# Performance work log

Hardware: AMD Instinct MI355X
Metric: run time of the kernel (lower is better)

## Reference

```python
import jax, jax.numpy as jnp
import numpy as np

MODEL_DIM = 2048
NUM_HEADS = 16
NUM_KV_HEADS = 4
HEAD_DIM = MODEL_DIM // NUM_HEADS  # 128
ROPE_BASE = 10000.0
LOCAL_WINDOW = 1024
EPS = 1.1920929e-07  # torch.finfo(float32).eps, F.rms_norm default
NEG = -1e30


def setup_inputs() -> dict:
    key = jax.random.key(0)
    ks = jax.random.split(key, 5)
    s = 0.02
    return {
        "x": jax.random.normal(ks[0], (1, 4096, MODEL_DIM), jnp.float32),
        "Wq": jax.random.normal(ks[1], (MODEL_DIM, MODEL_DIM), jnp.float32) * s,
        "Wk": jax.random.normal(ks[2], (NUM_KV_HEADS * HEAD_DIM, MODEL_DIM), jnp.float32) * s,
        "Wv": jax.random.normal(ks[3], (NUM_KV_HEADS * HEAD_DIM, MODEL_DIM), jnp.float32) * s,
        "Wo": jax.random.normal(ks[4], (MODEL_DIM, MODEL_DIM), jnp.float32) * s,
    }


def _rms_norm(x):
    return x * jax.lax.rsqrt(jnp.mean(x * x, axis=-1, keepdims=True) + EPS)


def _rope_tables(seqlen, dtype):
    inv_freq = 1.0 / (ROPE_BASE ** (jnp.arange(0, HEAD_DIM, 2, dtype=jnp.float32) / HEAD_DIM))
    freqs = jnp.arange(seqlen, dtype=jnp.float32)[:, None] * inv_freq[None, :]  # [S, hd/2]
    return jnp.cos(freqs).astype(dtype), jnp.sin(freqs).astype(dtype)


def _apply_rope(x, cos, sin):
    # x: [B, H, S, hd]; cos/sin: [S, hd/2]
    half = x.shape[-1] // 2
    x1, x2 = x[..., :half], x[..., half:]
    c = cos[None, None, :, :]
    s = sin[None, None, :, :]
    return jnp.concatenate((x1 * c + x2 * s, x2 * c - x1 * s), axis=-1)


def reference(x, Wq, Wk, Wv, Wo):
    B, S, _ = x.shape
    G = NUM_HEADS // NUM_KV_HEADS
    q = (x @ Wq.T).reshape(B, S, NUM_HEADS, HEAD_DIM).transpose(0, 2, 1, 3)
    k = (x @ Wk.T).reshape(B, S, NUM_KV_HEADS, HEAD_DIM).transpose(0, 2, 1, 3)
    v = (x @ Wv.T).reshape(B, S, NUM_KV_HEADS, HEAD_DIM).transpose(0, 2, 1, 3)
    q = _rms_norm(q)
    k = _rms_norm(k)
    cos, sin = _rope_tables(S, q.dtype)
    q = _apply_rope(q, cos, sin)
    k = _apply_rope(k, cos, sin)
    # GQA: expand kv heads to match query heads
    k = jnp.repeat(k, G, axis=1)  # [B, H, S, hd]
    v = jnp.repeat(v, G, axis=1)
    scale = 1.0 / np.sqrt(HEAD_DIM)
    scores = jnp.einsum("bhqd,bhkd->bhqk", q, k) * scale  # [B, H, S, S]
    idx = jnp.arange(S)
    causal = idx[None, :] <= idx[:, None]
    in_window = idx[None, :] > idx[:, None] - LOCAL_WINDOW
    allowed = causal & in_window  # [S, S]
    scores = jnp.where(allowed[None, None, :, :], scores, NEG)
    probs = jax.nn.softmax(scores, axis=-1)
    y = jnp.einsum("bhqk,bhkd->bhqd", probs, v)  # [B, H, S, hd]
    y = y.transpose(0, 2, 1, 3).reshape(B, S, MODEL_DIM)
    return y @ Wo.T
```

## Files before the change

### kernel.cpp

```cpp
#include <hip/hip_runtime.h>

typedef short bf16x8 __attribute__((ext_vector_type(8)));
typedef float f32x4 __attribute__((ext_vector_type(4)));

__device__ __forceinline__ ushort f2b(float f) {
  union { float f; unsigned u; } v; v.f = f;
  unsigned r = v.u + 0x7FFF + ((v.u >> 16) & 1);
  return (ushort)(r >> 16);
}
__device__ __forceinline__ float b2f(ushort u) {
  union { unsigned u; float f; } v; v.u = ((unsigned)u) << 16;
  return v.f;
}
__device__ __forceinline__ unsigned cvtpk(float lo, float hi) {
  unsigned r;
  asm volatile("v_cvt_pk_bf16_f32 %0, %1, %2" : "=v"(r) : "v"(lo), "v"(hi));
  return r;
}
__device__ __forceinline__ f32x4 mfma16(bf16x8 a, bf16x8 b, f32x4 c) {
  return __builtin_amdgcn_mfma_f32_16x16x32_bf16(a, b, c, 0, 0, 0);
}

#define GLD_LDS16(g, l) \
  __builtin_amdgcn_global_load_lds((const __attribute__((address_space(1))) void*)(g), \
                                   (__attribute__((address_space(3))) void*)(l), 16, 0, 0)

__global__ __launch_bounds__(256) void cast_bf16(const float* __restrict__ in,
                                                 ushort* __restrict__ out, int n4) {
  int i = blockIdx.x * 256 + threadIdx.x;
  if (i >= n4) return;
  float4 f = ((const float4*)in)[i];
  ushort4 u;
  u.x = f2b(f.x); u.y = f2b(f.y); u.z = f2b(f.z); u.w = f2b(f.w);
  ((ushort4*)out)[i] = u;
}

__global__ void rope_tables_k(float* __restrict__ cosT, float* __restrict__ sinT) {
  int s = blockIdx.x, i = threadIdx.x;
  float inv = powf(10000.0f, -(float)i * (1.0f / 64.0f));
  float f = (float)s * inv;
  cosT[s * 64 + i] = cosf(f);
  sinT[s * 64 + i] = sinf(f);
}

template <int BM, int BN, bool BF16OUT>
__global__ __launch_bounds__(512, 2) void gemm8p(const ushort* __restrict__ A,
                                                 const ushort* __restrict__ B,
                                                 void* __restrict__ Cout,
                                                 int M, int N, int K) {
  constexpr int AF = BM / 64;
  constexpr int BF = BN / 64;
  constexpr int MFR = BM / 32;
  constexpr int LA = BM / 128;
  constexpr int LB = BN / 128;
  constexpr int ASZ = BM * 32;
  constexpr int BSZ = BN * 32;
  __shared__ __align__(16) ushort lds[4 * (ASZ + BSZ)];
  const int t = threadIdx.x;
  const int lane = t & 63, w = t >> 6;
  const int wr = w & 1, wc = w >> 1;
  const int l15 = lane & 15, l4 = lane >> 4;
  const int nbn = N / BN;
  const int nwg = (int)gridDim.x;
  int bid = (int)blockIdx.x;
  bid = (bid & 7) * (nwg >> 3) + (bid >> 3);
  const long m0 = (long)(bid / nbn) * BM;
  const long n0 = (long)(bid % nbn) * BN;
  const int nk = K >> 6;
  const int rdl = (l4 * 16 + l15) * 8;

  f32x4 acc[MFR][BF] = {};
  bf16x8 af[AF], bf[BF];

#define STA(tile, ks)                                                          \
  do {                                                                         \
    const int tt_ = (tile) < nk ? (tile) : nk - 1;                             \
    _Pragma("unroll") for (int c = 0; c < LA; ++c) {                           \
      const int us_ = t * 8 + c * 4096;                                        \
      const int row_ = (us_ >> 9) * 16 + ((us_ >> 3) & 15);                    \
      const int col_ = ((us_ >> 7) & 3) * 8;                                   \
      GLD_LDS16(A + (m0 + row_) * K + tt_ * 64 + (ks) * 32 + col_,             \
                &lds[(((tile) & 1) * 2 + (ks)) * ASZ + us_]);                  \
    }                                                                          \
  } while (0)
#define STB(tile, ks)                                                          \
  do {                                                                         \
    const int tt_ = (tile) < nk ? (tile) : nk - 1;                             \
    _Pragma("unroll") for (int c = 0; c < LB; ++c) {                           \
      const int us_ = t * 8 + c * 4096;                                        \
      const int row_ = (us_ >> 9) * 16 + ((us_ >> 3) & 15);                    \
      const int col_ = ((us_ >> 7) & 3) * 8;                                   \
      GLD_LDS16(B + (n0 + row_) * K + tt_ * 64 + (ks) * 32 + col_,             \
                &lds[4 * ASZ + (((tile) & 1) * 2 + (ks)) * BSZ + us_]);        \
    }                                                                          \
  } while (0)
#define LDA8(slot, ks, mq)                                                     \
  _Pragma("unroll") for (int a = 0; a < AF; ++a)                               \
      af[a] = *(const bf16x8*)(&lds[((slot) * 2 + (ks)) * ASZ +                \
                                    (wr * MFR + (mq) * AF + a) * 512 + rdl]);
#define LDB8(slot, ks)                                                         \
  _Pragma("unroll") for (int b = 0; b < BF; ++b)                               \
      bf[b] = *(const bf16x8*)(&lds[4 * ASZ + ((slot) * 2 + (ks)) * BSZ +      \
                                    (wc * BF + b) * 512 + rdl]);
#define VMW()                                                                  \
  do {                                                                         \
    if constexpr (LA + 2 * LB == 6)                                            \
      asm volatile("s_waitcnt vmcnt(6)" ::: "memory");                         \
    else                                                                       \
      asm volatile("s_waitcnt vmcnt(5)" ::: "memory");                         \
  } while (0)
#define BARMM(mq)                                                              \
  do {                                                                         \
    __builtin_amdgcn_s_barrier();                                              \
    asm volatile("s_waitcnt lgkmcnt(0)" ::: "memory");                         \
    __builtin_amdgcn_sched_barrier(0);                                         \
    __builtin_amdgcn_s_setprio(1);                                             \
    _Pragma("unroll") for (int a = 0; a < AF; ++a)                             \
        _Pragma("unroll") for (int b = 0; b < BF; ++b)                         \
            acc[(mq) * AF + a][b] = mfma16(af[a], bf[b], acc[(mq) * AF + a][b]); \
    __builtin_amdgcn_s_setprio(0);                                             \
    __builtin_amdgcn_s_barrier();                                              \
  } while (0)

  STA(0, 0); STB(0, 0); STA(0, 1); STB(0, 1);
  STA(1, 0); STB(1, 0); STB(1, 1);
  VMW();
  __builtin_amdgcn_s_barrier();

  for (int i = 0; i < (nk >> 1); ++i) {
    const int t1 = 2 * i + 1, t2 = 2 * i + 2, t3 = 2 * i + 3;
    LDA8(0, 0, 0); LDB8(0, 0); STA(t1, 1);          BARMM(0);
    LDA8(0, 0, 1);             STB(t2, 0);          BARMM(1);
    LDA8(0, 1, 0); LDB8(0, 1); STA(t2, 0);          BARMM(0);
    LDA8(0, 1, 1);             STB(t2, 1); VMW();   BARMM(1);
    LDA8(1, 0, 0); LDB8(1, 0); STA(t2, 1);          BARMM(0);
    LDA8(1, 0, 1);             STB(t3, 0);          BARMM(1);
    LDA8(1, 1, 0); LDB8(1, 1); STA(t3, 0);          BARMM(0);
    LDA8(1, 1, 1);             STB(t3, 1); VMW();   BARMM(1);
  }
  asm volatile("s_waitcnt vmcnt(0)" ::: "memory");

#pragma unroll
  for (int m = 0; m < MFR; ++m) {
#pragma unroll
    for (int n = 0; n < BF; ++n) {
      long mrow = m0 + wr * (BM / 2) + m * 16 + l4 * 4;
      long ncol = n0 + wc * (BN / 4) + n * 16 + l15;
#pragma unroll
      for (int r = 0; r < 4; ++r) {
        if constexpr (BF16OUT)
          ((ushort*)Cout)[(mrow + r) * N + ncol] = f2b(acc[m][n][r]);
        else
          ((float*)Cout)[(mrow + r) * N + ncol] = acc[m][n][r];
      }
    }
  }
#undef STA
#undef STB
#undef LDA8
#undef LDB8
#undef VMW
#undef BARMM
}

__global__ __launch_bounds__(256) void postproc_k(const ushort* __restrict__ qkvb,
                                                  const float* __restrict__ cosT,
                                                  const float* __restrict__ sinT,
                                                  ushort* __restrict__ qb,
                                                  ushort* __restrict__ kb,
                                                  ushort* __restrict__ vtb) {
  const int lane = threadIdx.x & 63;
  const int s = blockIdx.x * 4 + (threadIdx.x >> 6);
  const int h = blockIdx.y;
  const int colbase = (h < 16) ? h * 128 : (h < 20 ? 2048 + (h - 16) * 128
                                                   : 2560 + (h - 20) * 128);
  const ushort* row = qkvb + (long)s * 3072 + colbase;
  float x1 = b2f(row[lane]), x2 = b2f(row[lane + 64]);
  if (h >= 20) {
    int kvh = h - 20;
    int spos = (s & ~31) | (((s >> 2) & 3) * 8 + ((s >> 4) & 1) * 4 + (s & 3));
    vtb[(long)(kvh * 128 + lane) * 4096 + spos]      = f2b(x1);
    vtb[(long)(kvh * 128 + lane + 64) * 4096 + spos] = f2b(x2);
    return;
  }
  float ss = x1 * x1 + x2 * x2;
#pragma unroll
  for (int m = 1; m < 64; m <<= 1) ss += __shfl_xor(ss, m);
  float rn = rsqrtf(ss * (1.0f / 128.0f) + 1.1920929e-07f);
  float c = cosT[s * 64 + lane], sn = sinT[s * 64 + lane];
  float x1n = x1 * rn, x2n = x2 * rn;
  float o1 = x1n * c + x2n * sn;
  float o2 = x2n * c - x1n * sn;
  if (h < 16) {
    const float scq = 0.08838834764831845f;
    ushort* dst = qb + ((long)h * 4096 + s) * 128;
    dst[lane] = f2b(o1 * scq);
    dst[lane + 64] = f2b(o2 * scq);
  } else {
    ushort* dst = kb + ((long)(h - 16) * 4096 + s) * 128;
    dst[lane] = f2b(o1);
    dst[lane + 64] = f2b(o2);
  }
}

__global__ __launch_bounds__(512) void attn_k(const ushort* __restrict__ qb,
                                              const ushort* __restrict__ kb,
                                              const ushort* __restrict__ vtb,
                                              ushort* __restrict__ yb) {
  __shared__ __align__(16) ushort lds[32768];
  const int t = threadIdx.x;
  const int lane = t & 63, w = t >> 6;
  const int l15 = lane & 15, l4 = lane >> 4;
  const int q0 = ((int)gridDim.x - 1 - (int)blockIdx.x) * 128;
  const int h = blockIdx.y, kvh = h >> 2;
  const int qw = q0 + w * 16;
  const int q = qw + l15;

  const ushort* Qp = qb + ((long)h * 4096 + q) * 128 + l4 * 8;
  bf16x8 qf[4];
#pragma unroll
  for (int c = 0; c < 4; ++c) qf[c] = *(const bf16x8*)(Qp + c * 32);

  const ushort* Kg = kb + (long)kvh * 4096 * 128;
  const ushort* Vg = vtb + (long)kvh * 128 * 4096;

  int kb_lo = q0 - 1023; if (kb_lo < 0) kb_lo = 0; kb_lo &= ~63;
  const int nt = (q0 + 127 - kb_lo) / 64 + 1;

  const int lbuA = w * 512 + lane * 8;
  const int lbuB = lbuA + 4096;
  const int krA = ((lbuA >> 9) >> 2) * 16 + ((lbuA >> 3) & 15);
  const int kcA = ((lbuA >> 9) & 3) * 32 + ((lbuA >> 7) & 3) * 8;
  const int krB = ((lbuB >> 9) >> 2) * 16 + ((lbuB >> 3) & 15);
  const int kcB = ((lbuB >> 9) & 3) * 32 + ((lbuB >> 7) & 3) * 8;
  const int vrA = ((lbuA >> 9) >> 1) * 16 + ((lbuA >> 5) & 15);
  const int vcA = ((lbuA >> 9) & 1) * 32 + ((lbuA >> 3) & 3) * 8;
  const int vrB = ((lbuB >> 9) >> 1) * 16 + ((lbuB >> 5) & 15);
  const int vcB = ((lbuB >> 9) & 1) * 32 + ((lbuB >> 3) & 3) * 8;

#define STAGE(kbs, b)                                                        \
  do {                                                                       \
    ushort* Kl_ = &lds[(b) * 16384];                                         \
    ushort* Vl_ = &lds[(b) * 16384 + 8192];                                  \
    GLD_LDS16(Kg + (long)((kbs) + krA) * 128 + kcA, Kl_ + lbuA);             \
    GLD_LDS16(Kg + (long)((kbs) + krB) * 128 + kcB, Kl_ + lbuB);             \
    GLD_LDS16(Vg + (long)vrA * 4096 + (kbs) + vcA, Vl_ + lbuA);              \
    GLD_LDS16(Vg + (long)vrB * 4096 + (kbs) + vcB, Vl_ + lbuB);              \
  } while (0)

  f32x4 o[8] = {};
  float mrun = -1e30f, lrun = 0.0f;

  STAGE(kb_lo, 0);
  asm volatile("s_waitcnt vmcnt(0)" ::: "memory");
  __syncthreads();

  for (int ti = 0; ti < nt; ++ti) {
    const int kbs = kb_lo + ti * 64;
    const int cur = ti & 1;
    if (ti + 1 < nt) STAGE(kbs + 64, cur ^ 1);

    if (kbs + 63 >= qw - 1023 && kbs <= qw + 15) {
      const ushort* Kl = &lds[cur * 16384];
      const ushort* Vl = &lds[cur * 16384 + 8192];
      const int rdl = (l4 * 16 + l15) * 8;

      f32x4 sc[4];
#pragma unroll
      for (int st = 0; st < 4; ++st) {
        sc[st] = f32x4{0.f, 0.f, 0.f, 0.f};
#pragma unroll
        for (int c = 0; c < 4; ++c)
          sc[st] = mfma16(*(const bf16x8*)(Kl + (st * 4 + c) * 512 + rdl),
                          qf[c], sc[st]);
      }

      const bool full = (kbs + 64 <= qw) && (kbs >= qw - 1008);
      float s[16];
      if (full) {
#pragma unroll
        for (int st = 0; st < 4; ++st)
#pragma unroll
          for (int r = 0; r < 4; ++r) s[st * 4 + r] = sc[st][r];
      } else {
#pragma unroll
        for (int st = 0; st < 4; ++st)
#pragma unroll
          for (int r = 0; r < 4; ++r) {
            const int ki = kbs + st * 16 + l4 * 4 + r;
            s[st * 4 + r] = (ki <= q && ki > q - 1024) ? sc[st][r] : -1e30f;
          }
      }

      float m0a = fmaxf(fmaxf(s[0], s[1]), fmaxf(s[2], s[3]));
      float m1a = fmaxf(fmaxf(s[4], s[5]), fmaxf(s[6], s[7]));
      float m2a = fmaxf(fmaxf(s[8], s[9]), fmaxf(s[10], s[11]));
      float m3a = fmaxf(fmaxf(s[12], s[13]), fmaxf(s[14], s[15]));
      float mx = fmaxf(fmaxf(m0a, m1a), fmaxf(m2a, m3a));
      mx = fmaxf(mx, __shfl_xor(mx, 16));
      mx = fmaxf(mx, __shfl_xor(mx, 32));

      float mn;
      if (__all(mx <= mrun + 8.0f)) {
        mn = mrun;
      } else {
        mn = fmaxf(mrun, mx);
        const float corr = __expf(mrun - mn);
        mrun = mn;
#pragma unroll
        for (int db = 0; db < 8; ++db)
#pragma unroll
          for (int r = 0; r < 4; ++r) o[db][r] *= corr;
        lrun *= corr;
      }

      float p[16];
#pragma unroll
      for (int j = 0; j < 16; ++j) p[j] = __expf(s[j] - mn);
      float ps = ((p[0] + p[1]) + (p[2] + p[3])) + ((p[4] + p[5]) + (p[6] + p[7]));
      ps += ((p[8] + p[9]) + (p[10] + p[11])) + ((p[12] + p[13]) + (p[14] + p[15]));
      ps += __shfl_xor(ps, 16);
      ps += __shfl_xor(ps, 32);
      lrun += ps;

      union { unsigned u[4]; bf16x8 v; } pa, pb;
      pa.u[0] = cvtpk(p[0], p[1]);   pa.u[1] = cvtpk(p[2], p[3]);
      pa.u[2] = cvtpk(p[4], p[5]);   pa.u[3] = cvtpk(p[6], p[7]);
      pb.u[0] = cvtpk(p[8], p[9]);   pb.u[1] = cvtpk(p[10], p[11]);
      pb.u[2] = cvtpk(p[12], p[13]); pb.u[3] = cvtpk(p[14], p[15]);

      const int vbase = l15 * 32 + l4 * 8;
#pragma unroll
      for (int db = 0; db < 8; ++db) {
        const ushort* vrp = Vl + db * 1024 + vbase;
        o[db] = mfma16(*(const bf16x8*)vrp, pa.v, o[db]);
        o[db] = mfma16(*(const bf16x8*)(vrp + 512), pb.v, o[db]);
      }
    }
    __syncthreads();
  }

  const float inv = 1.0f / lrun;
#pragma unroll
  for (int db = 0; db < 8; ++db)
#pragma unroll
    for (int r = 0; r < 4; ++r)
      yb[(long)q * 2048 + h * 128 + db * 16 + l4 * 4 + r] = f2b(o[db][r] * inv);
}

extern "C" void kernel_launch(void* const* d_in, const int* in_sizes, int n_in,
                              void* d_out, int out_size, void* d_ws, size_t ws_size,
                              hipStream_t stream) {
  (void)in_sizes; (void)n_in; (void)out_size; (void)ws_size;
  const float* x  = (const float*)d_in[0];
  const float* Wq = (const float*)d_in[1];
  const float* Wk = (const float*)d_in[2];
  const float* Wv = (const float*)d_in[3];
  const float* Wo = (const float*)d_in[4];
  const long S = 4096;
  ushort* ws   = (ushort*)d_ws;
  ushort* xb   = ws;
  ushort* wqkv = xb + S * 2048;
  ushort* wob  = wqkv + 3072L * 2048;
  ushort* qkvb = wob + 2048L * 2048;
  ushort* qb   = qkvb + S * 3072;
  ushort* kbuf = qb + S * 2048;
  ushort* vtb  = kbuf + 4L * 4096 * 128;
  ushort* yb   = vtb + 4L * 128 * 4096;
  float* cosT  = (float*)(yb + S * 2048);
  float* sinT  = cosT + S * 64;

  cast_bf16<<<dim3(8192), 256, 0, stream>>>(x, xb, (int)(S * 2048 / 4));
  cast_bf16<<<dim3(4096), 256, 0, stream>>>(Wq, wqkv, 2048 * 2048 / 4);
  cast_bf16<<<dim3(1024), 256, 0, stream>>>(Wk, wqkv + 2048L * 2048, 512 * 2048 / 4);
  cast_bf16<<<dim3(1024), 256, 0, stream>>>(Wv, wqkv + 2560L * 2048, 512 * 2048 / 4);
  cast_bf16<<<dim3(4096), 256, 0, stream>>>(Wo, wob, 2048 * 2048 / 4);

  gemm8p<256, 256, true><<<dim3(192), 512, 0, stream>>>(xb, wqkv, qkvb, 4096, 3072, 2048);
  rope_tables_k<<<dim3(4096), 64, 0, stream>>>(cosT, sinT);
  postproc_k<<<dim3(1024, 24), 256, 0, stream>>>(qkvb, cosT, sinT, qb, kbuf, vtb);
  attn_k<<<dim3(32, 16), 512, 0, stream>>>(qb, kbuf, vtb, yb);
  gemm8p<128, 256, false><<<dim3(256), 512, 0, stream>>>(yb, wob, d_out, 4096, 2048, 2048);
}
```

Measured before the change: 225.1 us.

## Fuse casts, simplify GEMM LDS layout, process two query tiles per attention wave

The five fp32-to-bf16 cast launches become one kernel that branches on index range, removing launch overhead. The GEMM global-to-LDS staging switches to a plain row-major 32-column layout with matching fragment read offsets. The attention kernel now runs 4 waves of 256 threads, each handling 32 queries as two 16-row groups. Each K/V fragment read from LDS therefore feeds two MFMAs, and two blocks per CU are requested. This doubles per-wave accumulator registers and may add LDS bank conflicts from the simpler layout.

New measurement: 201.6 us. 10.4% less time.

```diff
diff --git a/kernel.cpp b/kernel.cpp
--- a/kernel.cpp
+++ b/kernel.cpp
@@ -25,14 +25,33 @@
   __builtin_amdgcn_global_load_lds((const __attribute__((address_space(1))) void*)(g), \
                                    (__attribute__((address_space(3))) void*)(l), 16, 0, 0)
 
-__global__ __launch_bounds__(256) void cast_bf16(const float* __restrict__ in,
-                                                 ushort* __restrict__ out, int n4) {
-  int i = blockIdx.x * 256 + threadIdx.x;
-  if (i >= n4) return;
-  float4 f = ((const float4*)in)[i];
+__global__ __launch_bounds__(256) void cast_all(const float* __restrict__ x,
+                                                const float* __restrict__ wq,
+                                                const float* __restrict__ wk,
+                                                const float* __restrict__ wv,
+                                                const float* __restrict__ wo,
+                                                ushort* __restrict__ xb,
+                                                ushort* __restrict__ wqkvb,
+                                                ushort* __restrict__ wob) {
+  const long i = (long)blockIdx.x * 256 + threadIdx.x;
+  const float* src;
+  ushort* dst;
+  long j;
+  if (i < 2097152) {
+    src = x; j = i; dst = xb;
+  } else if (i < 3145728) {
+    src = wq; j = i - 2097152; dst = wqkvb;
+  } else if (i < 3407872) {
+    src = wk; j = i - 3145728; dst = wqkvb + 4194304;
+  } else if (i < 3670016) {
+    src = wv; j = i - 3407872; dst = wqkvb + 5242880;
+  } else {
+    src = wo; j = i - 3670016; dst = wob;
+  }
+  float4 f = ((const float4*)src)[j];
   ushort4 u;
   u.x = f2b(f.x); u.y = f2b(f.y); u.z = f2b(f.z); u.w = f2b(f.w);
-  ((ushort4*)out)[i] = u;
+  ((ushort4*)dst)[j] = u;
 }
 
 __global__ void rope_tables_k(float* __restrict__ cosT, float* __restrict__ sinT) {
@@ -67,7 +86,7 @@
   const long m0 = (long)(bid / nbn) * BM;
   const long n0 = (long)(bid % nbn) * BN;
   const int nk = K >> 6;
-  const int rdl = (l4 * 16 + l15) * 8;
+  const int rdl = l15 * 32 + l4 * 8;
 
   f32x4 acc[MFR][BF] = {};
   bf16x8 af[AF], bf[BF];
@@ -77,9 +96,7 @@
     const int tt_ = (tile) < nk ? (tile) : nk - 1;                             \
     _Pragma("unroll") for (int c = 0; c < LA; ++c) {                           \
       const int us_ = t * 8 + c * 4096;                                        \
-      const int row_ = (us_ >> 9) * 16 + ((us_ >> 3) & 15);                    \
-      const int col_ = ((us_ >> 7) & 3) * 8;                                   \
-      GLD_LDS16(A + (m0 + row_) * K + tt_ * 64 + (ks) * 32 + col_,             \
+      GLD_LDS16(A + (m0 + (us_ >> 5)) * K + tt_ * 64 + (ks) * 32 + (us_ & 31), \
                 &lds[(((tile) & 1) * 2 + (ks)) * ASZ + us_]);                  \
     }                                                                          \
   } while (0)
@@ -88,9 +105,7 @@
     const int tt_ = (tile) < nk ? (tile) : nk - 1;                             \
     _Pragma("unroll") for (int c = 0; c < LB; ++c) {                           \
       const int us_ = t * 8 + c * 4096;                                        \
-      const int row_ = (us_ >> 9) * 16 + ((us_ >> 3) & 15);                    \
-      const int col_ = ((us_ >> 7) & 3) * 8;                                   \
-      GLD_LDS16(B + (n0 + row_) * K + tt_ * 64 + (ks) * 32 + col_,             \
+      GLD_LDS16(B + (n0 + (us_ >> 5)) * K + tt_ * 64 + (ks) * 32 + (us_ & 31), \
                 &lds[4 * ASZ + (((tile) & 1) * 2 + (ks)) * BSZ + us_]);        \
     }                                                                          \
   } while (0)
@@ -203,23 +218,30 @@
   }
 }
 
-__global__ __launch_bounds__(512) void attn_k(const ushort* __restrict__ qb,
-                                              const ushort* __restrict__ kb,
-                                              const ushort* __restrict__ vtb,
-                                              ushort* __restrict__ yb) {
+__global__ __launch_bounds__(256, 2) void attn_k(const ushort* __restrict__ qb,
+                                                 const ushort* __restrict__ kb,
+                                                 const ushort* __restrict__ vtb,
+                                                 ushort* __restrict__ yb) {
   __shared__ __align__(16) ushort lds[32768];
   const int t = threadIdx.x;
   const int lane = t & 63, w = t >> 6;
   const int l15 = lane & 15, l4 = lane >> 4;
   const int q0 = ((int)gridDim.x - 1 - (int)blockIdx.x) * 128;
   const int h = blockIdx.y, kvh = h >> 2;
-  const int qw = q0 + w * 16;
-  const int q = qw + l15;
-
-  const ushort* Qp = qb + ((long)h * 4096 + q) * 128 + l4 * 8;
-  bf16x8 qf[4];
-#pragma unroll
-  for (int c = 0; c < 4; ++c) qf[c] = *(const bf16x8*)(Qp + c * 32);
+  const int qw = q0 + w * 32;
+  const int qA = qw + l15, qB = qw + 16 + l15;
+  const int lrd = l15 * 32 + l4 * 8;
+
+  bf16x8 qf0[4], qf1[4];
+  {
+    const ushort* QpA = qb + ((long)h * 4096 + qA) * 128 + l4 * 8;
+    const ushort* QpB = qb + ((long)h * 4096 + qB) * 128 + l4 * 8;
+#pragma unroll
+    for (int c = 0; c < 4; ++c) {
+      qf0[c] = *(const bf16x8*)(QpA + c * 32);
+      qf1[c] = *(const bf16x8*)(QpB + c * 32);
+    }
+  }
 
   const ushort* Kg = kb + (long)kvh * 4096 * 128;
   const ushort* Vg = vtb + (long)kvh * 128 * 4096;
@@ -227,29 +249,58 @@
   int kb_lo = q0 - 1023; if (kb_lo < 0) kb_lo = 0; kb_lo &= ~63;
   const int nt = (q0 + 127 - kb_lo) / 64 + 1;
 
-  const int lbuA = w * 512 + lane * 8;
-  const int lbuB = lbuA + 4096;
-  const int krA = ((lbuA >> 9) >> 2) * 16 + ((lbuA >> 3) & 15);
-  const int kcA = ((lbuA >> 9) & 3) * 32 + ((lbuA >> 7) & 3) * 8;
-  const int krB = ((lbuB >> 9) >> 2) * 16 + ((lbuB >> 3) & 15);
-  const int kcB = ((lbuB >> 9) & 3) * 32 + ((lbuB >> 7) & 3) * 8;
-  const int vrA = ((lbuA >> 9) >> 1) * 16 + ((lbuA >> 5) & 15);
-  const int vcA = ((lbuA >> 9) & 1) * 32 + ((lbuA >> 3) & 3) * 8;
-  const int vrB = ((lbuB >> 9) >> 1) * 16 + ((lbuB >> 5) & 15);
-  const int vcB = ((lbuB >> 9) & 1) * 32 + ((lbuB >> 3) & 3) * 8;
-
-#define STAGE(kbs, b)                                                        \
-  do {                                                                       \
-    ushort* Kl_ = &lds[(b) * 16384];                                         \
-    ushort* Vl_ = &lds[(b) * 16384 + 8192];                                  \
-    GLD_LDS16(Kg + (long)((kbs) + krA) * 128 + kcA, Kl_ + lbuA);             \
-    GLD_LDS16(Kg + (long)((kbs) + krB) * 128 + kcB, Kl_ + lbuB);             \
-    GLD_LDS16(Vg + (long)vrA * 4096 + (kbs) + vcA, Vl_ + lbuA);              \
-    GLD_LDS16(Vg + (long)vrB * 4096 + (kbs) + vcB, Vl_ + lbuB);              \
-  } while (0)
-
-  f32x4 o[8] = {};
-  float mrun = -1e30f, lrun = 0.0f;
+#define STAGE(kbs, b)                                                          \
+  do {                                                                         \
+    ushort* L_ = &lds[(b) * 16384];                                            \
+    _Pragma("unroll") for (int c = 0; c < 8; ++c) {                            \
+      const int us_ = t * 8 + c * 2048;                                        \
+      if (c < 4) {                                                             \
+        GLD_LDS16(Kg + (long)((kbs) + ((us_ >> 5) & 63)) * 128 +               \
+                      (us_ >> 11) * 32 + (us_ & 31),                           \
+                  L_ + us_);                                                   \
+      } else {                                                                 \
+        const int uv_ = us_ - 8192;                                            \
+        GLD_LDS16(Vg + (long)((uv_ >> 5) & 127) * 4096 + (kbs) +               \
+                      (uv_ >> 12) * 32 + (uv_ & 31),                           \
+                  L_ + us_);                                                   \
+      }                                                                        \
+    }                                                                          \
+  } while (0)
+
+#define SMAX(sg, mr, lr, og, PA, PB)                                           \
+  do {                                                                         \
+    float mx = fmaxf(fmaxf(fmaxf(sg[0], sg[1]), fmaxf(sg[2], sg[3])),          \
+                     fmaxf(fmaxf(sg[4], sg[5]), fmaxf(sg[6], sg[7])));         \
+    mx = fmaxf(mx, fmaxf(fmaxf(fmaxf(sg[8], sg[9]), fmaxf(sg[10], sg[11])),    \
+                         fmaxf(fmaxf(sg[12], sg[13]), fmaxf(sg[14], sg[15]))));\
+    mx = fmaxf(mx, __shfl_xor(mx, 16));                                        \
+    mx = fmaxf(mx, __shfl_xor(mx, 32));                                        \
+    float mn;                                                                  \
+    if (__all(mx <= (mr) + 8.0f)) {                                            \
+      mn = (mr);                                                               \
+    } else {                                                                   \
+      mn = fmaxf((mr), mx);                                                    \
+      const float corr = __expf((mr)-mn);                                      \
+      (mr) = mn;                                                               \
+      _Pragma("unroll") for (int db = 0; db < 8; ++db)                         \
+          _Pragma("unroll") for (int r = 0; r < 4; ++r) og[db][r] *= corr;     \
+      (lr) *= corr;                                                            \
+    }                                                                          \
+    float p[16];                                                               \
+    _Pragma("unroll") for (int j = 0; j < 16; ++j) p[j] = __expf(sg[j] - mn);  \
+    float ps = ((p[0] + p[1]) + (p[2] + p[3])) + ((p[4] + p[5]) + (p[6] + p[7])); \
+    ps += ((p[8] + p[9]) + (p[10] + p[11])) + ((p[12] + p[13]) + (p[14] + p[15])); \
+    ps += __shfl_xor(ps, 16);                                                  \
+    ps += __shfl_xor(ps, 32);                                                  \
+    (lr) += ps;                                                                \
+    PA.u[0] = cvtpk(p[0], p[1]);   PA.u[1] = cvtpk(p[2], p[3]);                \
+    PA.u[2] = cvtpk(p[4], p[5]);   PA.u[3] = cvtpk(p[6], p[7]);                \
+    PB.u[0] = cvtpk(p[8], p[9]);   PB.u[1] = cvtpk(p[10], p[11]);              \
+    PB.u[2] = cvtpk(p[12], p[13]); PB.u[3] = cvtpk(p[14], p[15]);              \
+  } while (0)
+
+  f32x4 o0[8] = {}, o1[8] = {};
+  float mr0 = -1e30f, lr0 = 0.0f, mr1 = -1e30f, lr1 = 0.0f;
 
   STAGE(kb_lo, 0);
   asm volatile("s_waitcnt vmcnt(0)" ::: "memory");
@@ -260,92 +311,82 @@
     const int cur = ti & 1;
     if (ti + 1 < nt) STAGE(kbs + 64, cur ^ 1);
 
-    if (kbs + 63 >= qw - 1023 && kbs <= qw + 15) {
+    if (kbs <= qw + 31 && kbs + 63 >= qw - 1023) {
       const ushort* Kl = &lds[cur * 16384];
-      const ushort* Vl = &lds[cur * 16384 + 8192];
-      const int rdl = (l4 * 16 + l15) * 8;
-
-      f32x4 sc[4];
+      const ushort* Vl = Kl + 8192;
+
+      f32x4 sc0[4], sc1[4];
 #pragma unroll
       for (int st = 0; st < 4; ++st) {
-        sc[st] = f32x4{0.f, 0.f, 0.f, 0.f};
-#pragma unroll
-        for (int c = 0; c < 4; ++c)
-          sc[st] = mfma16(*(const bf16x8*)(Kl + (st * 4 + c) * 512 + rdl),
-                          qf[c], sc[st]);
+        sc0[st] = f32x4{0.f, 0.f, 0.f, 0.f};
+        sc1[st] = f32x4{0.f, 0.f, 0.f, 0.f};
+#pragma unroll
+        for (int c = 0; c < 4; ++c) {
+          bf16x8 kf = *(const bf16x8*)(Kl + c * 2048 + st * 512 + lrd);
+          sc0[st] = mfma16(kf, qf0[c], sc0[st]);
+          sc1[st] = mfma16(kf, qf1[c], sc1[st]);
+        }
       }
 
-      const bool full = (kbs + 64 <= qw) && (kbs >= qw - 1008);
-      float s[16];
-      if (full) {
+      float s0[16], s1[16];
+      const bool fullA = (kbs + 64 <= qw) && (kbs >= qw - 1008);
+      const bool fullB = (kbs + 64 <= qw + 16) && (kbs >= qw - 992);
+      if (fullA) {
 #pragma unroll
         for (int st = 0; st < 4; ++st)
 #pragma unroll
-          for (int r = 0; r < 4; ++r) s[st * 4 + r] = sc[st][r];
+          for (int r = 0; r < 4; ++r) s0[st * 4 + r] = sc0[st][r];
       } else {
 #pragma unroll
         for (int st = 0; st < 4; ++st)
 #pragma unroll
           for (int r = 0; r < 4; ++r) {
             const int ki = kbs + st * 16 + l4 * 4 + r;
-            s[st * 4 + r] = (ki <= q && ki > q - 1024) ? sc[st][r] : -1e30f;
+            s0[st * 4 + r] = (ki <= qA && ki > qA - 1024) ? sc0[st][r] : -1e30f;
           }
       }
-
-      float m0a = fmaxf(fmaxf(s[0], s[1]), fmaxf(s[2], s[3]));
-      float m1a = fmaxf(fmaxf(s[4], s[5]), fmaxf(s[6], s[7]));
-      float m2a = fmaxf(fmaxf(s[8], s[9]), fmaxf(s[10], s[11]));
-      float m3a = fmaxf(fmaxf(s[12], s[13]), fmaxf(s[14], s[15]));
-      float mx = fmaxf(fmaxf(m0a, m1a), fmaxf(m2a, m3a));
-      mx = fmaxf(mx, __shfl_xor(mx, 16));
-      mx = fmaxf(mx, __shfl_xor(mx, 32));
-
-      float mn;
-      if (__all(mx <= mrun + 8.0f)) {
-        mn = mrun;
+      if (fullB) {
+#pragma unroll
+        for (int st = 0; st < 4; ++st)
+#pragma unroll
+          for (int r = 0; r < 4; ++r) s1[st * 4 + r] = sc1[st][r];
       } else {
-        mn = fmaxf(mrun, mx);
-        const float corr = __expf(mrun - mn);
-        mrun = mn;
-#pragma unroll
-        for (int db = 0; db < 8; ++db)
-#pragma unroll
-          for (int r = 0; r < 4; ++r) o[db][r] *= corr;
-        lrun *= corr;
+#pragma unroll
+        for (int st = 0; st < 4; ++st)
+#pragma unroll
+          for (int r = 0; r < 4; ++r) {
+            const int ki = kbs + st * 16 + l4 * 4 + r;
+            s1[st * 4 + r] = (ki <= qB && ki > qB - 1024) ? sc1[st][r] : -1e30f;
+          }
       }
 
-      float p[16];
-#pragma unroll
-      for (int j = 0; j < 16; ++j) p[j] = __expf(s[j] - mn);
-      float ps = ((p[0] + p[1]) + (p[2] + p[3])) + ((p[4] + p[5]) + (p[6] + p[7]));
-      ps += ((p[8] + p[9]) + (p[10] + p[11])) + ((p[12] + p[13]) + (p[14] + p[15]));
-      ps += __shfl_xor(ps, 16);
-      ps += __shfl_xor(ps, 32);
-      lrun += ps;
-
-      union { unsigned u[4]; bf16x8 v; } pa, pb;
-      pa.u[0] = cvtpk(p[0], p[1]);   pa.u[1] = cvtpk(p[2], p[3]);
-      pa.u[2] = cvtpk(p[4], p[5]);   pa.u[3] = cvtpk(p[6], p[7]);
-      pb.u[0] = cvtpk(p[8], p[9]);   pb.u[1] = cvtpk(p[10], p[11]);
-      pb.u[2] = cvtpk(p[12], p[13]); pb.u[3] = cvtpk(p[14], p[15]);
-
-      const int vbase = l15 * 32 + l4 * 8;
+      union { unsigned u[4]; bf16x8 v; } pa0, pb0, pa1, pb1;
+      SMAX(s0, mr0, lr0, o0, pa0, pb0);
+      SMAX(s1, mr1, lr1, o1, pa1, pb1);
+
 #pragma unroll
       for (int db = 0; db < 8; ++db) {
-        const ushort* vrp = Vl + db * 1024 + vbase;
-        o[db] = mfma16(*(const bf16x8*)vrp, pa.v, o[db]);
-        o[db] = mfma16(*(const bf16x8*)(vrp + 512), pb.v, o[db]);
+        bf16x8 v0 = *(const bf16x8*)(Vl + db * 512 + lrd);
+        o0[db] = mfma16(v0, pa0.v, o0[db]);
+        o1[db] = mfma16(v0, pa1.v, o1[db]);
+        bf16x8 v1 = *(const bf16x8*)(Vl + 4096 + db * 512 + lrd);
+        o0[db] = mfma16(v1, pb0.v, o0[db]);
+        o1[db] = mfma16(v1, pb1.v, o1[db]);
       }
     }
     __syncthreads();
   }
 
-  const float inv = 1.0f / lrun;
+  const float i0 = 1.0f / lr0, i1 = 1.0f / lr1;
 #pragma unroll
   for (int db = 0; db < 8; ++db)
 #pragma unroll
-    for (int r = 0; r < 4; ++r)
-      yb[(long)q * 2048 + h * 128 + db * 16 + l4 * 4 + r] = f2b(o[db][r] * inv);
+    for (int r = 0; r < 4; ++r) {
+      yb[(long)qA * 2048 + h * 128 + db * 16 + l4 * 4 + r] = f2b(o0[db][r] * i0);
+      yb[(long)qB * 2048 + h * 128 + db * 16 + l4 * 4 + r] = f2b(o1[db][r] * i1);
+    }
+#undef STAGE
+#undef SMAX
 }
 
 extern "C" void kernel_launch(void* const* d_in, const int* in_sizes, int n_in,
@@ -370,15 +411,10 @@
   float* cosT  = (float*)(yb + S * 2048);
   float* sinT  = cosT + S * 64;
 
-  cast_bf16<<<dim3(8192), 256, 0, stream>>>(x, xb, (int)(S * 2048 / 4));
-  cast_bf16<<<dim3(4096), 256, 0, stream>>>(Wq, wqkv, 2048 * 2048 / 4);
-  cast_bf16<<<dim3(1024), 256, 0, stream>>>(Wk, wqkv + 2048L * 2048, 512 * 2048 / 4);
-  cast_bf16<<<dim3(1024), 256, 0, stream>>>(Wv, wqkv + 2560L * 2048, 512 * 2048 / 4);
-  cast_bf16<<<dim3(4096), 256, 0, stream>>>(Wo, wob, 2048 * 2048 / 4);
-
+  cast_all<<<dim3(18432), 256, 0, stream>>>(x, Wq, Wk, Wv, Wo, xb, wqkv, wob);
   gemm8p<256, 256, true><<<dim3(192), 512, 0, stream>>>(xb, wqkv, qkvb, 4096, 3072, 2048);
   rope_tables_k<<<dim3(4096), 64, 0, stream>>>(cosT, sinT);
   postproc_k<<<dim3(1024, 24), 256, 0, stream>>>(qkvb, cosT, sinT, qb, kbuf, vtb);
-  attn_k<<<dim3(32, 16), 512, 0, stream>>>(qb, kbuf, vtb, yb);
+  attn_k<<<dim3(32, 16), 256, 0, stream>>>(qb, kbuf, vtb, yb);
   gemm8p<128, 256, false><<<dim3(256), 512, 0, stream>>>(yb, wob, d_out, 4096, 2048, 2048);
 }
```
